# Kernel optimization log

Measured on AMD Instinct MI355X. Metric: run time of the kernel, lower is better.

## Reference

```python
import jax, jax.numpy as jnp
import numpy as np

B, L, D, H, E = 64, 128, 768, 2, 131072  # graphs, nodes/graph, hidden, heads, edges
N = B * L
C = D // H  # per-head channels


def _transformer_conv(x, src, dst, wq, bq, wk, bk, wv, bv, ws, bs):
    # PyG TransformerConv (concat=True, root_weight=True, beta=False)
    n = x.shape[0]
    q = (x @ wq + bq).reshape(n, H, C)
    k = (x @ wk + bk).reshape(n, H, C)
    v = (x @ wv + bv).reshape(n, H, C)
    # per-edge attention logits [E, H]
    logits = jnp.sum(q[dst] * k[src], axis=-1) * (1.0 / np.sqrt(C))
    # scatter softmax over incoming edges of each dst node
    m = jax.ops.segment_max(logits, dst, num_segments=n)
    e = jnp.exp(logits - m[dst])
    s = jax.ops.segment_sum(e, dst, num_segments=n)
    alpha = e / s[dst]  # [E, H]
    msg = alpha[..., None] * v[src]  # [E, H, C]
    agg = jax.ops.segment_sum(msg, dst, num_segments=n).reshape(n, D)
    return agg + x @ ws + bs


def setup_inputs() -> dict:
    key = jax.random.key(0)
    ks = jax.random.split(key, 24)
    x = jax.random.normal(ks[0], (N, D), jnp.float32)
    # within-graph random edges
    dst = jax.random.randint(ks[1], (E,), 0, N)
    off = jax.random.randint(ks[2], (E,), 0, L)
    src = (dst // L) * L + off
    edge_index = jnp.stack([src, dst]).astype(jnp.int32)

    def lin(k, i, o):
        return jax.random.normal(k, (i, o), jnp.float32) * 0.02

    inp = {"x": x, "edge_index": edge_index}
    i = 3
    for layer in ("1", "2"):
        for nm in ("wq", "wk", "wv", "ws"):
            inp[nm + layer] = lin(ks[i], D, D); i += 1
            inp["b" + nm[1] + layer] = jnp.zeros((D,), jnp.float32)
    inp["atti_w"] = lin(ks[i], 2 * D, D); i += 1
    inp["atti_b"] = jnp.zeros((D,), jnp.float32)
    inp["atts_w"] = lin(ks[i], D, 1); i += 1
    inp["atts_b"] = jnp.zeros((1,), jnp.float32)
    inp["fc1_w"] = lin(ks[i], D, D); i += 1
    inp["fc1_b"] = jnp.zeros((D,), jnp.float32)
    inp["fc2_w"] = lin(ks[i], D, 3); i += 1
    inp["fc2_b"] = jnp.zeros((3,), jnp.float32)
    return inp


def reference(x, edge_index, wq1, bq1, wk1, bk1, wv1, bv1, ws1, bs1,
              wq2, bq2, wk2, bk2, wv2, bv2, ws2, bs2,
              atti_w, atti_b, atts_w, atts_b, fc1_w, fc1_b, fc2_w, fc2_b):
    src, dst = edge_index[0], edge_index[1]
    h = jax.nn.relu(_transformer_conv(x, src, dst, wq1, bq1, wk1, bk1, wv1, bv1, ws1, bs1))
    h = jax.nn.relu(_transformer_conv(h, src, dst, wq2, bq2, wk2, bk2, wv2, bv2, ws2, bs2))
    # pad(): equal-size graphs -> reshape, mask all-valid (x_mask all False)
    hp = h.reshape(B, L, D)
    # attention pooling (eval path): query = first node of each graph
    x_q = jnp.broadcast_to(hp[:, :1], hp.shape)  # [B, L, D]
    x_c = jax.nn.relu(jnp.concatenate([x_q, hp], axis=-1) @ atti_w + atti_b)
    score = x_c @ atts_w + atts_b  # [B, L, 1]
    score = jax.nn.softmax(score, axis=1)
    pooled = jnp.sum(hp * score, axis=1)  # [B, D]
    out = jnp.tanh(pooled @ fc1_w + fc1_b) @ fc2_w + fc2_b
    return jax.nn.log_softmax(out, axis=-1)
```

## Files before the change

### kernel.cpp

```cpp
#include <hip/hip_runtime.h>

#define NN 8192
#define DD 768
#define EE 131072
#define BBg 64
#define LLn 128
#define CCh 384

typedef unsigned short u16;
typedef unsigned char u8;
typedef __attribute__((ext_vector_type(8))) short short8;
typedef __attribute__((ext_vector_type(4))) float f32x4;

__device__ __forceinline__ float b2f(u16 u) {
    union { unsigned int i; float f; } x; x.i = ((unsigned int)u) << 16; return x.f;
}
__device__ __forceinline__ u16 f2b(float f) {
    union { float f; unsigned int i; } x; x.f = f;
    unsigned int r = x.i + 0x7fffu + ((x.i >> 16) & 1u);
    return (u16)(r >> 16);
}
__device__ __forceinline__ void gload16(const void* g, void* l) {
    __builtin_amdgcn_global_load_lds((const __attribute__((address_space(1))) void*)g,
                                     (__attribute__((address_space(3))) void*)l, 16, 0, 0);
}

__global__ __launch_bounds__(256) void prep_kernel(const float* __restrict__ in,
                                                   u16* __restrict__ out,
                                                   unsigned int* __restrict__ cnt32,
                                                   float* __restrict__ score) {
    int i = blockIdx.x * 256 + threadIdx.x;
    float4 v = ((const float4*)in)[i];
    ushort4 o; o.x = f2b(v.x); o.y = f2b(v.y); o.z = f2b(v.z); o.w = f2b(v.w);
    ((ushort4*)out)[i] = o;
    if (blockIdx.x < 1024) cnt32[i] = 0;
    else if (blockIdx.x < 1056) score[i - 1024 * 256] = 0.f;
}

struct TP { const float* src; u16* dst; int rowOff; };
struct TP11 { TP a[11]; };

__global__ __launch_bounds__(256) void combo_kernel(TP11 args,
                                                    const int* __restrict__ srcp,
                                                    const int* __restrict__ dstp,
                                                    unsigned int* __restrict__ cnt32) {
    __shared__ float tile[64][65];
    if (blockIdx.z == 11) {
        for (int e = blockIdx.x * 256 + threadIdx.x; e < EE; e += 144 * 256) {
            int d = dstp[e], s = srcp[e];
            int g = d >> 7;
            int idx = (g << 14) + ((d & 127) << 7) + (s & 127);
            atomicAdd(&cnt32[idx >> 2], 1u << ((idx & 3) * 8));
        }
        return;
    }
    TP tp = args.a[blockIdx.z];
    int bx = blockIdx.x % 12, by = blockIdx.x / 12;
    int n0 = bx * 64, k0 = by * 64;
    int t = threadIdx.x;
    int tc = t & 63, tr = t >> 6;
#pragma unroll
    for (int i = 0; i < 16; i++)
        tile[tr + i * 4][tc] = tp.src[(size_t)(tp.rowOff + k0 + tr + i * 4) * DD + n0 + tc];
    __syncthreads();
#pragma unroll
    for (int i = 0; i < 16; i++) {
        int row = tr + i * 4;
        tp.dst[(size_t)(n0 + row) * DD + k0 + tc] = f2b(tile[tc][row]);
    }
}

enum { EPI_F32 = 1, EPI_TANH = 3 };

__global__ __launch_bounds__(256) void gemm_bf16(const u16* __restrict__ A,
                                                 const u16* __restrict__ Wt,
                                                 const float* __restrict__ bias,
                                                 void* __restrict__ outp, int K, int mode) {
    __shared__ u16 As[64][72];
    __shared__ u16 Bs[64][72];
    const int m0 = blockIdx.y * 64, n0 = blockIdx.x * 64;
    const int t = threadIdx.x;
    const int lane = t & 63, w = t >> 6;
    const int tr = t >> 2, tc = (t & 3) * 16;
    f32x4 acc[4] = {{0,0,0,0},{0,0,0,0},{0,0,0,0},{0,0,0,0}};
    const int fRow = lane & 15;
    const int fK = (lane >> 4) * 8;

    for (int k0 = 0; k0 < K; k0 += 64) {
        int4 a0 = *(const int4*)(A + (size_t)(m0 + tr) * K + k0 + tc);
        int4 a1 = *(const int4*)(A + (size_t)(m0 + tr) * K + k0 + tc + 8);
        int4 b0 = *(const int4*)(Wt + (size_t)(n0 + tr) * K + k0 + tc);
        int4 b1 = *(const int4*)(Wt + (size_t)(n0 + tr) * K + k0 + tc + 8);
        __syncthreads();
        *(int4*)&As[tr][tc] = a0; *(int4*)&As[tr][tc + 8] = a1;
        *(int4*)&Bs[tr][tc] = b0; *(int4*)&Bs[tr][tc + 8] = b1;
        __syncthreads();
#pragma unroll
        for (int s = 0; s < 2; s++) {
            short8 af = *(const short8*)&As[w * 16 + fRow][s * 32 + fK];
#pragma unroll
            for (int g = 0; g < 4; g++) {
                short8 bf = *(const short8*)&Bs[g * 16 + fRow][s * 32 + fK];
                acc[g] = __builtin_amdgcn_mfma_f32_16x16x32_bf16(af, bf, acc[g], 0, 0, 0);
            }
        }
    }
    const int colLocal = lane & 15;
    const int rowLocal = (lane >> 4) * 4;
#pragma unroll
    for (int g = 0; g < 4; g++) {
        int col = n0 + g * 16 + colLocal;
        float bv = bias ? bias[col] : 0.f;
#pragma unroll
        for (int i = 0; i < 4; i++) {
            int row = m0 + w * 16 + rowLocal + i;
            float v = acc[g][i] + bv;
            if (mode == EPI_TANH) v = tanhf(v);
            ((float*)outp)[(size_t)row * DD + col] = v;
        }
    }
}

#define SLAB 24576
__global__ __launch_bounds__(512, 2) void gemm256(const u16* __restrict__ A,
                                                  const u16* __restrict__ Wt,
                                                  const float* __restrict__ b0,
                                                  const float* __restrict__ b1,
                                                  const float* __restrict__ b2,
                                                  const float* __restrict__ b3,
                                                  u16* __restrict__ o0, u16* __restrict__ o1,
                                                  u16* __restrict__ o2, u16* __restrict__ o3) {
    __shared__ u16 smem[3 * SLAB];
    const int K = DD;
    const int t = threadIdx.x;
    const int lane = t & 63, w = t >> 6;
    const int wr = w >> 1, wc = w & 1;
    const int id = blockIdx.y * 24 + blockIdx.x;
    const int xcd = id & 7, jj = id >> 3;
    const int by = (xcd >> 1) * 8 + jj / 12;
    const int bx = (xcd & 1) * 12 + jj % 12;
    const int m0 = by * 256, n0 = bx * 128;
    const int fRow = lane & 15, fThr = lane >> 4;
    const u16* Abase = A + (size_t)m0 * K;
    const u16* Bbase = Wt + (size_t)n0 * K;

    auto stage = [&](u16* slab, int kt2) {
        const int k0 = kt2 * 64;
#pragma unroll
        for (int s = 0; s < 4; ++s) {
            int c = t + 512 * s;
            int row = c >> 3;
            int col = ((c & 7) ^ (row & 7)) * 8;
            gload16(Abase + (size_t)row * K + k0 + col, (char*)slab + (size_t)c * 16);
        }
#pragma unroll
        for (int s = 0; s < 2; ++s) {
            int c = t + 512 * s;
            int row = c >> 3;
            int col = ((c & 7) ^ (row & 7)) * 8;
            gload16(Bbase + (size_t)row * K + k0 + col, (char*)(slab + 16384) + (size_t)c * 16);
        }
    };
    auto loadFrags = [&](const u16* As, const u16* Bs, int p, short8* af, short8* bf) {
        const int cj = p * 4 + fThr;
#pragma unroll
        for (int i = 0; i < 4; ++i) {
            const int R = wr * 64 + i * 16 + fRow;
            af[i] = *(const short8*)&As[((size_t)R * 8 + (cj ^ (R & 7))) * 8];
        }
#pragma unroll
        for (int g = 0; g < 4; ++g) {
            const int Rb = wc * 64 + g * 16 + fRow;
            bf[g] = *(const short8*)&Bs[((size_t)Rb * 8 + (cj ^ (Rb & 7))) * 8];
        }
    };

    stage(smem, 0);
    stage(smem + SLAB, 1);
    asm volatile("s_waitcnt vmcnt(6)" ::: "memory");
    __builtin_amdgcn_s_barrier();

    short8 afA[4], bfA[4], afB[4], bfB[4];
    loadFrags(smem, smem + 16384, 0, afA, bfA);

    f32x4 acc[4][4] = {};
    int cur = 0;
    for (int kt = 0; kt < 12; ++kt) {
        const u16* As = smem + cur * SLAB;
        const u16* Bs = As + 16384;
        int nx = cur + 2; if (nx >= 3) nx -= 3;
        int pv = cur + 1; if (pv >= 3) pv -= 3;
        if (kt < 10) stage(smem + nx * SLAB, kt + 2);

        loadFrags(As, Bs, 1, afB, bfB);
        asm volatile("s_waitcnt lgkmcnt(8)" ::: "memory");
        __builtin_amdgcn_sched_barrier(0);
        __builtin_amdgcn_s_setprio(1);
#pragma unroll
        for (int i = 0; i < 4; ++i)
#pragma unroll
            for (int g = 0; g < 4; ++g)
                acc[i][g] = __builtin_amdgcn_mfma_f32_16x16x32_bf16(afA[i], bfA[g], acc[i][g], 0, 0, 0);
        __builtin_amdgcn_s_setprio(0);

        if (kt < 10) asm volatile("s_waitcnt vmcnt(6)" ::: "memory");
        else         asm volatile("s_waitcnt vmcnt(0)" ::: "memory");
        __builtin_amdgcn_s_barrier();

        if (kt < 11) {
            loadFrags(smem + pv * SLAB, smem + pv * SLAB + 16384, 0, afA, bfA);
            asm volatile("s_waitcnt lgkmcnt(8)" ::: "memory");
        } else {
            asm volatile("s_waitcnt lgkmcnt(0)" ::: "memory");
        }
        __builtin_amdgcn_sched_barrier(0);
        __builtin_amdgcn_s_setprio(1);
#pragma unroll
        for (int i = 0; i < 4; ++i)
#pragma unroll
            for (int g = 0; g < 4; ++g)
                acc[i][g] = __builtin_amdgcn_mfma_f32_16x16x32_bf16(afB[i], bfB[g], acc[i][g], 0, 0, 0);
        __builtin_amdgcn_s_setprio(0);
        __builtin_amdgcn_s_barrier();

        cur = pv;
    }

    const int chunk = n0 / DD;
    const float* bp = (chunk == 0) ? b0 : (chunk == 1) ? b1 : (chunk == 2) ? b2 : b3;
    u16* op = (chunk == 0) ? o0 : (chunk == 1) ? o1 : (chunk == 2) ? o2 : o3;
    const int cb0 = n0 - chunk * DD;
    if (chunk == 2) {
        u16 (*Vt)[264] = (u16(*)[264])smem;
#pragma unroll
        for (int g = 0; g < 4; g++) {
            float bv = bp[cb0 + wc * 64 + g * 16 + fRow];
#pragma unroll
            for (int i = 0; i < 4; i++)
#pragma unroll
                for (int rr = 0; rr < 4; rr++)
                    Vt[wc * 64 + g * 16 + fRow][wr * 64 + i * 16 + fThr * 4 + rr] =
                        f2b(acc[i][g][rr] + bv);
        }
        __syncthreads();
#pragma unroll
        for (int ii = 0; ii < 16; ii++) {
            int c = t + 512 * ii;
            int col = c >> 6, ch = c & 63;
            *(ushort4*)(op + (size_t)(cb0 + col) * NN + m0 + ch * 4) =
                *(const ushort4*)&Vt[col][ch * 4];
        }
    } else {
        u16 (*Cs)[136] = (u16(*)[136])smem;
#pragma unroll
        for (int g = 0; g < 4; g++) {
            float bv = bp[cb0 + wc * 64 + g * 16 + fRow];
#pragma unroll
            for (int i = 0; i < 4; i++)
#pragma unroll
                for (int rr = 0; rr < 4; rr++)
                    Cs[wr * 64 + i * 16 + fThr * 4 + rr][wc * 64 + g * 16 + fRow] =
                        f2b(acc[i][g][rr] + bv);
        }
        __syncthreads();
#pragma unroll
        for (int ii = 0; ii < 16; ii++) {
            int c = t + 512 * ii;
            int row = c >> 5, ch = c & 31;
            *(ushort4*)(op + (size_t)(m0 + row) * DD + cb0 + ch * 4) =
                *(const ushort4*)&Cs[row][ch * 4];
        }
    }
}

__global__ __launch_bounds__(256) void gemm_xc(const u16* __restrict__ A,
                                               const u16* __restrict__ Wt,
                                               const u16* __restrict__ wt8,
                                               const float* __restrict__ atti_b,
                                               const float* __restrict__ atts_w,
                                               float* __restrict__ score) {
    __shared__ u16 As[128 * 64];
    __shared__ u16 Bs[128 * 64];
    __shared__ float aq_p[2][128];
    const int K = DD;
    const int t = threadIdx.x;
    const int lane = t & 63, w = t >> 6;
    const int wr = w >> 1, wc = w & 1;
    const int n0 = blockIdx.x * 128, m0 = blockIdx.y * 128;
    const int fRow = lane & 15, fThr = lane >> 4;

    {
        int col = t & 127, kh = t >> 7;
        const u16* xr = A + (size_t)m0 * DD + kh * 384;
        const u16* wr8 = wt8 + (size_t)(n0 + col) * DD + kh * 384;
        float s = 0.f;
#pragma unroll 8
        for (int j = 0; j < 96; j++) {
            ushort4 a4 = *(const ushort4*)(xr + j * 4);
            ushort4 b4 = *(const ushort4*)(wr8 + j * 4);
            s += b2f(a4.x) * b2f(b4.x) + b2f(a4.y) * b2f(b4.y)
               + b2f(a4.z) * b2f(b4.z) + b2f(a4.w) * b2f(b4.w);
        }
        aq_p[kh][col] = s;
    }

    f32x4 acc[4][4] = {};
    const u16* Abase = A + (size_t)m0 * K;
    const u16* Bbase = Wt + (size_t)n0 * K;
    for (int k0 = 0; k0 < K; k0 += 64) {
        __syncthreads();
#pragma unroll
        for (int i = 0; i < 4; i++) {
            int c = t + 256 * i;
            int row = c >> 3;
            int col = ((c & 7) ^ (row & 7)) * 8;
            gload16(Abase + (size_t)row * K + k0 + col, (char*)As + (size_t)c * 16);
            gload16(Bbase + (size_t)row * K + k0 + col, (char*)Bs + (size_t)c * 16);
        }
        __syncthreads();
#pragma unroll
        for (int kk = 0; kk < 64; kk += 32) {
            const int cjW = (kk >> 3) + fThr;
            short8 af[4], bf[4];
#pragma unroll
            for (int i = 0; i < 4; i++) {
                int R = wr * 64 + i * 16 + fRow;
                af[i] = *(const short8*)&As[(R * 8 + (cjW ^ (R & 7))) * 8];
            }
#pragma unroll
            for (int g = 0; g < 4; g++) {
                int R = wc * 64 + g * 16 + fRow;
                bf[g] = *(const short8*)&Bs[(R * 8 + (cjW ^ (R & 7))) * 8];
            }
#pragma unroll
            for (int i = 0; i < 4; i++)
#pragma unroll
                for (int g = 0; g < 4; g++)
                    acc[i][g] = __builtin_amdgcn_mfma_f32_16x16x32_bf16(af[i], bf[g], acc[i][g], 0, 0, 0);
        }
    }
    float rsum[4][4] = {};
#pragma unroll
    for (int g = 0; g < 4; g++) {
        int cl = wc * 64 + g * 16 + fRow;
        int col = n0 + cl;
        float bv = atti_b[col] + aq_p[0][cl] + aq_p[1][cl];
        float av = atts_w[col];
#pragma unroll
        for (int i = 0; i < 4; i++)
#pragma unroll
            for (int rr = 0; rr < 4; rr++) {
                float v = fmaxf(acc[i][g][rr] + bv, 0.f);
                rsum[i][rr] += v * av;
            }
    }
#pragma unroll
    for (int i = 0; i < 4; i++)
#pragma unroll
        for (int rr = 0; rr < 4; rr++) {
            float s = rsum[i][rr];
            s += __shfl_xor(s, 1, 16); s += __shfl_xor(s, 2, 16);
            s += __shfl_xor(s, 4, 16); s += __shfl_xor(s, 8, 16);
            if (fRow == 0)
                atomicAdd(&score[m0 + wr * 64 + i * 16 + fThr * 4 + rr], s);
        }
}

__global__ __launch_bounds__(256) void attn_fused(const u16* __restrict__ qb,
                                                  const u16* __restrict__ kb,
                                                  const u16* __restrict__ vT,
                                                  const u8* __restrict__ cnt,
                                                  const u16* __restrict__ hs,
                                                  u16* __restrict__ out) {
    __shared__ u16 As[64][72];
    __shared__ u16 Bs[128][72];
    __shared__ u16 Pl[64][136];
    __shared__ u16 Vt[64][136];
    const int half = blockIdx.x, hd = blockIdx.y, g = blockIdx.z;
    const int t = threadIdx.x;
    const int lane = t & 63, w = t >> 6;
    const int fRow = lane & 15, fThr = lane >> 4;
    const int dstBase = g * 128 + half * 64;
    const u16* Qb = qb + (size_t)dstBase * DD + hd * CCh;
    const u16* Kb = kb + (size_t)(g * 128) * DD + hd * CCh;

    f32x4 acc[8] = {};
    const int trA = t >> 2, tcA = (t & 3) * 16;
    const int trB = t >> 1, tcB = (t & 1) * 32;
    for (int k0 = 0; k0 < CCh; k0 += 64) {
        int4 a0 = *(const int4*)(Qb + (size_t)trA * DD + k0 + tcA);
        int4 a1 = *(const int4*)(Qb + (size_t)trA * DD + k0 + tcA + 8);
        int4 b0 = *(const int4*)(Kb + (size_t)trB * DD + k0 + tcB);
        int4 b1 = *(const int4*)(Kb + (size_t)trB * DD + k0 + tcB + 8);
        int4 b2 = *(const int4*)(Kb + (size_t)trB * DD + k0 + tcB + 16);
        int4 b3 = *(const int4*)(Kb + (size_t)trB * DD + k0 + tcB + 24);
        __syncthreads();
        *(int4*)&As[trA][tcA] = a0; *(int4*)&As[trA][tcA + 8] = a1;
        *(int4*)&Bs[trB][tcB] = b0; *(int4*)&Bs[trB][tcB + 8] = b1;
        *(int4*)&Bs[trB][tcB + 16] = b2; *(int4*)&Bs[trB][tcB + 24] = b3;
        __syncthreads();
#pragma unroll
        for (int kk = 0; kk < 64; kk += 32) {
            short8 af = *(const short8*)&As[w * 16 + fRow][kk + fThr * 8];
#pragma unroll
            for (int j = 0; j < 8; j++) {
                short8 bf = *(const short8*)&Bs[j * 16 + fRow][kk + fThr * 8];
                acc[j] = __builtin_amdgcn_mfma_f32_16x16x32_bf16(af, bf, acc[j], 0, 0, 0);
            }
        }
    }

    const float scale = 0.05103103630798288f;
    const u8* cg = cnt + ((size_t)g << 14);
    const int rbase = half * 64 + w * 16 + fThr * 4;
    float pv[8][4];
#pragma unroll
    for (int i = 0; i < 4; i++) {
        float m = -3.4e38f;
#pragma unroll
        for (int j = 0; j < 8; j++) {
            float c = (float)cg[(rbase + i) * 128 + j * 16 + fRow];
            float s = acc[j][i] * scale;
            pv[j][i] = c;
            if (c > 0.f) m = fmaxf(m, s);
        }
#pragma unroll
        for (int msk = 1; msk <= 8; msk <<= 1) m = fmaxf(m, __shfl_xor(m, msk, 16));
        float sum = 0.f;
#pragma unroll
        for (int j = 0; j < 8; j++) {
            float p = (pv[j][i] > 0.f) ? pv[j][i] * __expf(acc[j][i] * scale - m) : 0.f;
            pv[j][i] = p; sum += p;
        }
#pragma unroll
        for (int msk = 1; msk <= 8; msk <<= 1) sum += __shfl_xor(sum, msk, 16);
        float inv = (sum > 0.f) ? 1.f / sum : 0.f;
#pragma unroll
        for (int j = 0; j < 8; j++)
            Pl[w * 16 + fThr * 4 + i][j * 16 + fRow] = f2b(pv[j][i] * inv);
    }

    for (int cc = 0; cc < 6; cc++) {
        __syncthreads();
#pragma unroll
        for (int ii = 0; ii < 4; ii++) {
            int q = t + 256 * ii;
            int row = q >> 4, col = (q & 15) * 8;
            *(int4*)&Vt[row][col] =
                *(const int4*)(vT + (size_t)(hd * CCh + cc * 64 + row) * NN + g * 128 + col);
        }
        __syncthreads();
        f32x4 acc2[4] = {};
#pragma unroll
        for (int kk = 0; kk < 128; kk += 32) {
            short8 af = *(const short8*)&Pl[w * 16 + fRow][kk + fThr * 8];
#pragma unroll
            for (int j = 0; j < 4; j++) {
                short8 bf = *(const short8*)&Vt[j * 16 + fRow][kk + fThr * 8];
                acc2[j] = __builtin_amdgcn_mfma_f32_16x16x32_bf16(af, bf, acc2[j], 0, 0, 0);
            }
        }
#pragma unroll
        for (int j = 0; j < 4; j++) {
            int c = hd * CCh + cc * 64 + j * 16 + fRow;
#pragma unroll
            for (int i = 0; i < 4; i++) {
                int row = dstBase + w * 16 + fThr * 4 + i;
                size_t idx = (size_t)row * DD + c;
                float r = fmaxf(acc2[j][i] + b2f(hs[idx]), 0.f);
                out[idx] = f2b(r);
            }
        }
    }
}

__global__ __launch_bounds__(192) void pool_kernel(const float* __restrict__ score,
                                                   const u16* __restrict__ hx,
                                                   u16* __restrict__ pb) {
    int b = blockIdx.x, t = threadIdx.x;
    __shared__ float sprob[LLn];
    if (t < 64) {
        float s0 = score[b * LLn + t];
        float s1 = score[b * LLn + 64 + t];
        float mx = fmaxf(s0, s1);
#pragma unroll
        for (int m = 1; m <= 32; m <<= 1) mx = fmaxf(mx, __shfl_xor(mx, m, 64));
        float e0 = __expf(s0 - mx), e1 = __expf(s1 - mx);
        float sum = e0 + e1;
#pragma unroll
        for (int m = 1; m <= 32; m <<= 1) sum += __shfl_xor(sum, m, 64);
        float inv = 1.f / sum;
        sprob[t] = e0 * inv; sprob[t + 64] = e1 * inv;
    }
    __syncthreads();
    int c = t * 4;
    float a0 = 0, a1 = 0, a2 = 0, a3 = 0;
    for (int l = 0; l < LLn; l++) {
        float wl = sprob[l];
        ushort4 hv = *(const ushort4*)(hx + (size_t)(b * LLn + l) * DD + c);
        a0 += wl * b2f(hv.x); a1 += wl * b2f(hv.y); a2 += wl * b2f(hv.z); a3 += wl * b2f(hv.w);
    }
    ushort4 o; o.x = f2b(a0); o.y = f2b(a1); o.z = f2b(a2); o.w = f2b(a3);
    *(ushort4*)(pb + (size_t)b * DD + c) = o;
}

__global__ __launch_bounds__(256) void head2_kernel(const float* __restrict__ u,
                                                    const float* __restrict__ fc2w,
                                                    const float* __restrict__ fc2b,
                                                    float* __restrict__ outp) {
    int b = blockIdx.x, t = threadIdx.x;
    __shared__ float sred[4][3];
    float p0 = 0, p1 = 0, p2 = 0;
    for (int k = t; k < DD; k += 256) {
        float uv = u[(size_t)b * DD + k];
        p0 += uv * fc2w[k * 3 + 0]; p1 += uv * fc2w[k * 3 + 1]; p2 += uv * fc2w[k * 3 + 2];
    }
#pragma unroll
    for (int m = 1; m <= 32; m <<= 1) {
        p0 += __shfl_xor(p0, m, 64); p1 += __shfl_xor(p1, m, 64); p2 += __shfl_xor(p2, m, 64);
    }
    int w = t >> 6, lane = t & 63;
    if (lane == 0) { sred[w][0] = p0; sred[w][1] = p1; sred[w][2] = p2; }
    __syncthreads();
    if (t == 0) {
        float z0 = fc2b[0], z1 = fc2b[1], z2 = fc2b[2];
        for (int i = 0; i < 4; i++) { z0 += sred[i][0]; z1 += sred[i][1]; z2 += sred[i][2]; }
        float mx = fmaxf(z0, fmaxf(z1, z2));
        float lse = mx + logf(__expf(z0 - mx) + __expf(z1 - mx) + __expf(z2 - mx));
        outp[b * 3 + 0] = z0 - lse; outp[b * 3 + 1] = z1 - lse; outp[b * 3 + 2] = z2 - lse;
    }
}

static inline char* carve(char*& p, size_t bytes) {
    char* r = p;
    p += (bytes + 255) & ~(size_t)255;
    return r;
}

extern "C" void kernel_launch(void* const* d_in, const int* in_sizes, int n_in,
                              void* d_out, int out_size, void* d_ws, size_t ws_size,
                              hipStream_t stream) {
    const float* x = (const float*)d_in[0];
    const int* ei = (const int*)d_in[1];
    const int* srcp = ei;
    const int* dstp = ei + EE;
    const float* wL[8] = {(const float*)d_in[2], (const float*)d_in[4], (const float*)d_in[6],
                          (const float*)d_in[8], (const float*)d_in[10], (const float*)d_in[12],
                          (const float*)d_in[14], (const float*)d_in[16]};
    const float* bL[8] = {(const float*)d_in[3], (const float*)d_in[5], (const float*)d_in[7],
                          (const float*)d_in[9], (const float*)d_in[11], (const float*)d_in[13],
                          (const float*)d_in[15], (const float*)d_in[17]};
    const float* atti_w = (const float*)d_in[18];
    const float* atti_b = (const float*)d_in[19];
    const float* atts_w = (const float*)d_in[20];
    const float* fc1_w = (const float*)d_in[22];
    const float* fc1_b = (const float*)d_in[23];
    const float* fc2_w = (const float*)d_in[24];
    const float* fc2_b = (const float*)d_in[25];
    float* outp = (float*)d_out;

    char* p = (char*)d_ws;
    const size_t ndb = (size_t)NN * DD * 2;
    const size_t wsz = (size_t)DD * DD * 2;
    u16* qb = (u16*)carve(p, ndb);
    u16* kb = (u16*)carve(p, ndb);
    u16* vt = (u16*)carve(p, ndb);
    u16* xb = (u16*)carve(p, ndb);
    u16* hb = (u16*)carve(p, ndb);
    u16* hs = (u16*)carve(p, ndb);
    u16* wtcat1 = (u16*)carve(p, wsz * 4);
    u16* wtcat2 = (u16*)carve(p, wsz * 4);
    u16* wt8 = (u16*)carve(p, wsz);
    u16* wt9 = (u16*)carve(p, wsz);
    u16* wtfc1 = (u16*)carve(p, wsz);
    u16* pb = (u16*)carve(p, (size_t)BBg * DD * 2);
    float* uu = (float*)carve(p, (size_t)BBg * DD * 4);
    u8* cnt = (u8*)carve(p, (size_t)BBg * 128 * 128);
    float* score = (float*)carve(p, NN * 4);

    prep_kernel<<<6144, 256, 0, stream>>>(x, xb, (unsigned int*)cnt, score);

    TP11 tps;
    for (int i = 0; i < 4; i++) tps.a[i] = {wL[i], wtcat1 + (size_t)i * DD * DD, 0};
    for (int i = 0; i < 4; i++) tps.a[4 + i] = {wL[4 + i], wtcat2 + (size_t)i * DD * DD, 0};
    tps.a[8] = {atti_w, wt8, 0};
    tps.a[9] = {atti_w, wt9, DD};
    tps.a[10] = {fc1_w, wtfc1, 0};
    combo_kernel<<<dim3(144, 1, 12), 256, 0, stream>>>(tps, srcp, dstp, (unsigned int*)cnt);

    dim3 gf(24, 32);
    dim3 ga(2, 2, BBg);
    gemm256<<<gf, 512, 0, stream>>>(xb, wtcat1, bL[0], bL[1], bL[2], bL[3], qb, kb, vt, hs);
    attn_fused<<<ga, 256, 0, stream>>>(qb, kb, vt, cnt, hs, hb);
    gemm256<<<gf, 512, 0, stream>>>(hb, wtcat2, bL[4], bL[5], bL[6], bL[7], qb, kb, vt, hs);
    attn_fused<<<ga, 256, 0, stream>>>(qb, kb, vt, cnt, hs, xb);

    gemm_xc<<<dim3(6, 64), 256, 0, stream>>>(xb, wt9, wt8, atti_b, atts_w, score);

    pool_kernel<<<BBg, 192, 0, stream>>>(score, xb, pb);
    gemm_bf16<<<dim3(12, 1), 256, 0, stream>>>(pb, wtfc1, fc1_b, uu, DD, EPI_TANH);
    head2_kernel<<<BBg, 256, 0, stream>>>(uu, fc2_w, fc2_b, outp);
}
```

Measured before the change: 343.2 us.

## Split K across wave pairs in gemm256 with LDS cross-wave reduction

Reworks the projection GEMM so that each pair of waves splits the K dimension of every 64-wide tile instead of splitting the N columns. Each wave accumulates a 64x128 partial tile, and the two partials are summed through LDS before the bias and store epilogue. The global-to-LDS staging is split into two halves interleaved with the MFMA phases. This is meant to cut B-fragment LDS reads per MFMA and to overlap loads with compute better, at the cost of doubled accumulator registers (risking occupancy at 2 blocks per CU) and an extra LDS reduction pass.

Result: no change. 344.0 us (+0.2%).

```diff
diff --git a/kernel.cpp b/kernel.cpp
--- a/kernel.cpp
+++ b/kernel.cpp
@@ -134,7 +134,7 @@
     const int K = DD;
     const int t = threadIdx.x;
     const int lane = t & 63, w = t >> 6;
-    const int wr = w >> 1, wc = w & 1;
+    const int mrow = w >> 1, ks = w & 1;
     const int id = blockIdx.y * 24 + blockIdx.x;
     const int xcd = id & 7, jj = id >> 3;
     const int by = (xcd >> 1) * 8 + jj / 12;
@@ -144,87 +144,162 @@
     const u16* Abase = A + (size_t)m0 * K;
     const u16* Bbase = Wt + (size_t)n0 * K;
 
-    auto stage = [&](u16* slab, int kt2) {
-        const int k0 = kt2 * 64;
-#pragma unroll
-        for (int s = 0; s < 4; ++s) {
-            int c = t + 512 * s;
-            int row = c >> 3;
-            int col = ((c & 7) ^ (row & 7)) * 8;
-            gload16(Abase + (size_t)row * K + k0 + col, (char*)slab + (size_t)c * 16);
-        }
-#pragma unroll
-        for (int s = 0; s < 2; ++s) {
-            int c = t + 512 * s;
-            int row = c >> 3;
-            int col = ((c & 7) ^ (row & 7)) * 8;
-            gload16(Bbase + (size_t)row * K + k0 + col, (char*)(slab + 16384) + (size_t)c * 16);
+    auto stageH = [&](u16* slab, int ktS, int half) {
+        const int k0 = ktS * 64;
+        if (half == 0) {
+#pragma unroll
+            for (int s = 0; s < 3; ++s) {
+                int c = t + 512 * s;
+                int row = c >> 3, col = ((c & 7) ^ (row & 7)) * 8;
+                gload16(Abase + (size_t)row * K + k0 + col, (char*)slab + (size_t)c * 16);
+            }
+        } else {
+            {
+                int c = t + 512 * 3;
+                int row = c >> 3, col = ((c & 7) ^ (row & 7)) * 8;
+                gload16(Abase + (size_t)row * K + k0 + col, (char*)slab + (size_t)c * 16);
+            }
+#pragma unroll
+            for (int s = 0; s < 2; ++s) {
+                int c = t + 512 * s;
+                int row = c >> 3, col = ((c & 7) ^ (row & 7)) * 8;
+                gload16(Bbase + (size_t)row * K + k0 + col, (char*)(slab + 16384) + (size_t)c * 16);
+            }
         }
     };
-    auto loadFrags = [&](const u16* As, const u16* Bs, int p, short8* af, short8* bf) {
-        const int cj = p * 4 + fThr;
+    auto loadAB = [&](const u16* As, short8 (&af)[4], short8 (&bfLo)[4]) {
+        const u16* Bs = As + 16384;
+        const int cj = ks * 4 + fThr;
 #pragma unroll
         for (int i = 0; i < 4; ++i) {
-            const int R = wr * 64 + i * 16 + fRow;
+            int R = mrow * 64 + i * 16 + fRow;
             af[i] = *(const short8*)&As[((size_t)R * 8 + (cj ^ (R & 7))) * 8];
         }
 #pragma unroll
         for (int g = 0; g < 4; ++g) {
-            const int Rb = wc * 64 + g * 16 + fRow;
+            int Rb = g * 16 + fRow;
+            bfLo[g] = *(const short8*)&Bs[((size_t)Rb * 8 + (cj ^ (Rb & 7))) * 8];
+        }
+    };
+    auto loadHi = [&](const u16* As, short8 (&bf)[4]) {
+        const u16* Bs = As + 16384;
+        const int cj = ks * 4 + fThr;
+#pragma unroll
+        for (int g = 0; g < 4; ++g) {
+            int Rb = (g + 4) * 16 + fRow;
             bf[g] = *(const short8*)&Bs[((size_t)Rb * 8 + (cj ^ (Rb & 7))) * 8];
         }
     };
 
-    stage(smem, 0);
-    stage(smem + SLAB, 1);
-    asm volatile("s_waitcnt vmcnt(6)" ::: "memory");
-    __builtin_amdgcn_s_barrier();
-
-    short8 afA[4], bfA[4], afB[4], bfB[4];
-    loadFrags(smem, smem + 16384, 0, afA, bfA);
-
-    f32x4 acc[4][4] = {};
-    int cur = 0;
-    for (int kt = 0; kt < 12; ++kt) {
-        const u16* As = smem + cur * SLAB;
-        const u16* Bs = As + 16384;
-        int nx = cur + 2; if (nx >= 3) nx -= 3;
-        int pv = cur + 1; if (pv >= 3) pv -= 3;
-        if (kt < 10) stage(smem + nx * SLAB, kt + 2);
-
-        loadFrags(As, Bs, 1, afB, bfB);
-        asm volatile("s_waitcnt lgkmcnt(8)" ::: "memory");
+    f32x4 acc[4][8] = {};
+    auto mfmaLo = [&](short8 (&af)[4], short8 (&bf)[4]) {
+#pragma unroll
+        for (int i = 0; i < 4; ++i)
+#pragma unroll
+            for (int g = 0; g < 4; ++g)
+                acc[i][g] = __builtin_amdgcn_mfma_f32_16x16x32_bf16(af[i], bf[g], acc[i][g], 0, 0, 0);
+    };
+    auto mfmaHi = [&](short8 (&af)[4], short8 (&bf)[4]) {
+#pragma unroll
+        for (int i = 0; i < 4; ++i)
+#pragma unroll
+            for (int g = 0; g < 4; ++g)
+                acc[i][4 + g] = __builtin_amdgcn_mfma_f32_16x16x32_bf16(af[i], bf[g], acc[i][4 + g], 0, 0, 0);
+    };
+
+    short8 afP[4], bfLoP[4], afQ[4], bfLoQ[4], bfH[4];
+
+    auto tileStep = [&](const u16* As, const u16* AsN, u16* Sst,
+                        short8 (&af)[4], short8 (&bfLo)[4],
+                        short8 (&afN)[4], short8 (&bfLoN)[4], int kt) {
+        loadHi(As, bfH);
+        if (kt <= 9) stageH(Sst, kt + 2, 0);
+        asm volatile("s_waitcnt lgkmcnt(4)" ::: "memory");
         __builtin_amdgcn_sched_barrier(0);
         __builtin_amdgcn_s_setprio(1);
-#pragma unroll
-        for (int i = 0; i < 4; ++i)
-#pragma unroll
-            for (int g = 0; g < 4; ++g)
-                acc[i][g] = __builtin_amdgcn_mfma_f32_16x16x32_bf16(afA[i], bfA[g], acc[i][g], 0, 0, 0);
+        mfmaLo(af, bfLo);
         __builtin_amdgcn_s_setprio(0);
-
-        if (kt < 10) asm volatile("s_waitcnt vmcnt(6)" ::: "memory");
+        if (kt <= 9) asm volatile("s_waitcnt vmcnt(3)" ::: "memory");
         else         asm volatile("s_waitcnt vmcnt(0)" ::: "memory");
         __builtin_amdgcn_s_barrier();
-
-        if (kt < 11) {
-            loadFrags(smem + pv * SLAB, smem + pv * SLAB + 16384, 0, afA, bfA);
+        if (kt <= 10) {
+            loadAB(AsN, afN, bfLoN);
+            if (kt <= 9) stageH(Sst, kt + 2, 1);
             asm volatile("s_waitcnt lgkmcnt(8)" ::: "memory");
         } else {
             asm volatile("s_waitcnt lgkmcnt(0)" ::: "memory");
         }
         __builtin_amdgcn_sched_barrier(0);
         __builtin_amdgcn_s_setprio(1);
-#pragma unroll
-        for (int i = 0; i < 4; ++i)
-#pragma unroll
-            for (int g = 0; g < 4; ++g)
-                acc[i][g] = __builtin_amdgcn_mfma_f32_16x16x32_bf16(afB[i], bfB[g], acc[i][g], 0, 0, 0);
+        mfmaHi(af, bfH);
         __builtin_amdgcn_s_setprio(0);
         __builtin_amdgcn_s_barrier();
-
-        cur = pv;
-    }
+    };
+
+    stageH(smem, 0, 0); stageH(smem, 0, 1);
+    stageH(smem + SLAB, 1, 0); stageH(smem + SLAB, 1, 1);
+    asm volatile("s_waitcnt vmcnt(6)" ::: "memory");
+    __builtin_amdgcn_s_barrier();
+    loadAB(smem, afP, bfLoP);
+
+    int cur = 0;
+    for (int it = 0; it < 6; ++it) {
+        int s1 = cur + 1; if (s1 >= 3) s1 -= 3;
+        int s2 = cur + 2; if (s2 >= 3) s2 -= 3;
+        u16* S0 = smem + cur * SLAB;
+        u16* S1 = smem + s1 * SLAB;
+        u16* S2 = smem + s2 * SLAB;
+        tileStep(S0, S1, S2, afP, bfLoP, afQ, bfLoQ, 2 * it);
+        tileStep(S1, S2, S0, afQ, bfLoQ, afP, bfLoP, 2 * it + 1);
+        cur = s2;
+    }
+
+    char* xbuf = (char*)smem;
+    const int wreg = mrow * 2 + 1 - ks;
+    const int rreg = mrow * 2 + ks;
+    if (ks == 0) {
+#pragma unroll
+        for (int i = 0; i < 4; i++)
+#pragma unroll
+            for (int g = 0; g < 4; g++) {
+                int f = i * 4 + g;
+                int unit = lane * 16 + ((f + lane) & 15);
+                *(f32x4*)(xbuf + wreg * 16384 + unit * 16) = acc[i][4 + g];
+            }
+    } else {
+#pragma unroll
+        for (int i = 0; i < 4; i++)
+#pragma unroll
+            for (int g = 0; g < 4; g++) {
+                int f = i * 4 + g;
+                int unit = lane * 16 + ((f + lane) & 15);
+                *(f32x4*)(xbuf + wreg * 16384 + unit * 16) = acc[i][g];
+            }
+    }
+    __syncthreads();
+    f32x4 fin[4][4];
+    if (ks == 0) {
+#pragma unroll
+        for (int i = 0; i < 4; i++)
+#pragma unroll
+            for (int g = 0; g < 4; g++) {
+                int f = i * 4 + g;
+                int unit = lane * 16 + ((f + lane) & 15);
+                f32x4 p = *(const f32x4*)(xbuf + rreg * 16384 + unit * 16);
+                fin[i][g] = acc[i][g] + p;
+            }
+    } else {
+#pragma unroll
+        for (int i = 0; i < 4; i++)
+#pragma unroll
+            for (int g = 0; g < 4; g++) {
+                int f = i * 4 + g;
+                int unit = lane * 16 + ((f + lane) & 15);
+                f32x4 p = *(const f32x4*)(xbuf + rreg * 16384 + unit * 16);
+                fin[i][g] = acc[i][4 + g] + p;
+            }
+    }
+    __syncthreads();
 
     const int chunk = n0 / DD;
     const float* bp = (chunk == 0) ? b0 : (chunk == 1) ? b1 : (chunk == 2) ? b2 : b3;
@@ -234,13 +309,13 @@
         u16 (*Vt)[264] = (u16(*)[264])smem;
 #pragma unroll
         for (int g = 0; g < 4; g++) {
-            float bv = bp[cb0 + wc * 64 + g * 16 + fRow];
+            float bv = bp[cb0 + ks * 64 + g * 16 + fRow];
 #pragma unroll
             for (int i = 0; i < 4; i++)
 #pragma unroll
                 for (int rr = 0; rr < 4; rr++)
-                    Vt[wc * 64 + g * 16 + fRow][wr * 64 + i * 16 + fThr * 4 + rr] =
-                        f2b(acc[i][g][rr] + bv);
+                    Vt[ks * 64 + g * 16 + fRow][mrow * 64 + i * 16 + fThr * 4 + rr] =
+                        f2b(fin[i][g][rr] + bv);
         }
         __syncthreads();
 #pragma unroll
@@ -254,13 +329,13 @@
         u16 (*Cs)[136] = (u16(*)[136])smem;
 #pragma unroll
         for (int g = 0; g < 4; g++) {
-            float bv = bp[cb0 + wc * 64 + g * 16 + fRow];
+            float bv = bp[cb0 + ks * 64 + g * 16 + fRow];
 #pragma unroll
             for (int i = 0; i < 4; i++)
 #pragma unroll
                 for (int rr = 0; rr < 4; rr++)
-                    Cs[wr * 64 + i * 16 + fThr * 4 + rr][wc * 64 + g * 16 + fRow] =
-                        f2b(acc[i][g][rr] + bv);
+                    Cs[mrow * 64 + i * 16 + fThr * 4 + rr][ks * 64 + g * 16 + fRow] =
+                        f2b(fin[i][g][rr] + bv);
         }
         __syncthreads();
 #pragma unroll
```

## Enlarge QKVS GEMM tile to 256x256 with double-buffered quarter-step pipeline

Applied to the files above, without the earlier changes.

Changes the fused Q/K/V/skip projection GEMM from 256x128 output tiles with a triple-buffered K loop to 256x256 tiles. Each wave now owns 128x64 of the output, and the loads for the next K tile are split into four sub-stages interleaved with four MFMA sub-blocks over two shared-memory buffers. The larger tile raises arithmetic intensity and halves the number of blocks, from 768 to 384. In exchange, the 128 accumulator registers per thread add register pressure at 2 blocks/CU, there are more barriers per K step, and the epilogue now runs in two shared-memory passes.

Measured after the change: 368.5 us. 1.07x slower.

```diff
diff --git a/kernel.cpp b/kernel.cpp
--- a/kernel.cpp
+++ b/kernel.cpp
@@ -121,7 +121,7 @@
     }
 }
 
-#define SLAB 24576
+#define BUFU 32768
 __global__ __launch_bounds__(512, 2) void gemm256(const u16* __restrict__ A,
                                                   const u16* __restrict__ Wt,
                                                   const float* __restrict__ b0,
@@ -130,145 +130,192 @@
                                                   const float* __restrict__ b3,
                                                   u16* __restrict__ o0, u16* __restrict__ o1,
                                                   u16* __restrict__ o2, u16* __restrict__ o3) {
-    __shared__ u16 smem[3 * SLAB];
+    __shared__ u16 smem[2 * BUFU];
     const int K = DD;
     const int t = threadIdx.x;
     const int lane = t & 63, w = t >> 6;
-    const int wr = w >> 1, wc = w & 1;
-    const int id = blockIdx.y * 24 + blockIdx.x;
+    const int wm = w >> 2, wn = w & 3;
+    const int id = blockIdx.y * 12 + blockIdx.x;
     const int xcd = id & 7, jj = id >> 3;
-    const int by = (xcd >> 1) * 8 + jj / 12;
-    const int bx = (xcd & 1) * 12 + jj % 12;
-    const int m0 = by * 256, n0 = bx * 128;
+    const int by = xcd * 4 + jj / 12;
+    const int bx = jj % 12;
+    const int m0 = by * 256, n0 = bx * 256;
     const int fRow = lane & 15, fThr = lane >> 4;
     const u16* Abase = A + (size_t)m0 * K;
     const u16* Bbase = Wt + (size_t)n0 * K;
 
-    auto stage = [&](u16* slab, int kt2) {
-        const int k0 = kt2 * 64;
-#pragma unroll
-        for (int s = 0; s < 4; ++s) {
-            int c = t + 512 * s;
-            int row = c >> 3;
-            int col = ((c & 7) ^ (row & 7)) * 8;
-            gload16(Abase + (size_t)row * K + k0 + col, (char*)slab + (size_t)c * 16);
-        }
+    auto stageA = [&](int b, int kt, int h) {
+        const int k0 = kt * 64;
+        char* dst = (char*)(smem + b * BUFU);
 #pragma unroll
         for (int s = 0; s < 2; ++s) {
-            int c = t + 512 * s;
-            int row = c >> 3;
-            int col = ((c & 7) ^ (row & 7)) * 8;
-            gload16(Bbase + (size_t)row * K + k0 + col, (char*)(slab + 16384) + (size_t)c * 16);
+            int c = h * 1024 + t + 512 * s;
+            int row = c >> 3, col = ((c & 7) ^ (row & 7)) * 8;
+            gload16(Abase + (size_t)row * K + k0 + col, dst + (size_t)c * 16);
         }
     };
-    auto loadFrags = [&](const u16* As, const u16* Bs, int p, short8* af, short8* bf) {
-        const int cj = p * 4 + fThr;
-#pragma unroll
-        for (int i = 0; i < 4; ++i) {
-            const int R = wr * 64 + i * 16 + fRow;
-            af[i] = *(const short8*)&As[((size_t)R * 8 + (cj ^ (R & 7))) * 8];
-        }
-#pragma unroll
-        for (int g = 0; g < 4; ++g) {
-            const int Rb = wc * 64 + g * 16 + fRow;
-            bf[g] = *(const short8*)&Bs[((size_t)Rb * 8 + (cj ^ (Rb & 7))) * 8];
+    auto stageB = [&](int b, int kt, int h) {
+        const int k0 = kt * 64;
+        char* dst = (char*)(smem + b * BUFU + 16384);
+#pragma unroll
+        for (int s = 0; s < 2; ++s) {
+            int c = h * 1024 + t + 512 * s;
+            int row = c >> 3, col = ((c & 7) ^ (row & 7)) * 8;
+            gload16(Bbase + (size_t)row * K + k0 + col, dst + (size_t)c * 16);
         }
     };
 
-    stage(smem, 0);
-    stage(smem + SLAB, 1);
-    asm volatile("s_waitcnt vmcnt(6)" ::: "memory");
-    __builtin_amdgcn_s_barrier();
-
-    short8 afA[4], bfA[4], afB[4], bfB[4];
-    loadFrags(smem, smem + 16384, 0, afA, bfA);
-
-    f32x4 acc[4][4] = {};
-    int cur = 0;
-    for (int kt = 0; kt < 12; ++kt) {
-        const u16* As = smem + cur * SLAB;
-        const u16* Bs = As + 16384;
-        int nx = cur + 2; if (nx >= 3) nx -= 3;
-        int pv = cur + 1; if (pv >= 3) pv -= 3;
-        if (kt < 10) stage(smem + nx * SLAB, kt + 2);
-
-        loadFrags(As, Bs, 1, afB, bfB);
-        asm volatile("s_waitcnt lgkmcnt(8)" ::: "memory");
+    short8 fa[4][2], fb0[2][2], fb1[2][2];
+    f32x4 acc[8][4] = {};
+
+    auto loadA = [&](const u16* Ab, int ih) {
+#pragma unroll
+        for (int i = 0; i < 4; ++i)
+#pragma unroll
+            for (int kk = 0; kk < 2; ++kk) {
+                int R = wm * 128 + ih * 64 + i * 16 + fRow;
+                int cj = kk * 4 + fThr;
+                fa[i][kk] = *(const short8*)&Ab[((size_t)R * 8 + (cj ^ (R & 7))) * 8];
+            }
+    };
+    auto loadB = [&](const u16* Bb, int gh, short8 (&fb)[2][2]) {
+#pragma unroll
+        for (int g = 0; g < 2; ++g)
+#pragma unroll
+            for (int kk = 0; kk < 2; ++kk) {
+                int Rb = wn * 64 + gh * 32 + g * 16 + fRow;
+                int cj = kk * 4 + fThr;
+                fb[g][kk] = *(const short8*)&Bb[((size_t)Rb * 8 + (cj ^ (Rb & 7))) * 8];
+            }
+    };
+    auto mm = [&](int ibase, short8 (&fb)[2][2], int gbase) {
+#pragma unroll
+        for (int kk = 0; kk < 2; ++kk)
+#pragma unroll
+            for (int i = 0; i < 4; ++i)
+#pragma unroll
+                for (int g = 0; g < 2; ++g)
+                    acc[ibase + i][gbase + g] = __builtin_amdgcn_mfma_f32_16x16x32_bf16(
+                        fa[i][kk], fb[g][kk], acc[ibase + i][gbase + g], 0, 0, 0);
+    };
+
+    auto ktile4 = [&](int bufb, auto&& st1, auto&& st2, auto&& st3, auto&& st4, bool vm0end) {
+        const u16* Ab = smem + bufb * BUFU;
+        const u16* Bb = Ab + 16384;
+        loadA(Ab, 0);
+        loadB(Bb, 0, fb0);
+        st1();
+        __builtin_amdgcn_s_barrier();
+        asm volatile("s_waitcnt lgkmcnt(0)" ::: "memory");
         __builtin_amdgcn_sched_barrier(0);
         __builtin_amdgcn_s_setprio(1);
-#pragma unroll
-        for (int i = 0; i < 4; ++i)
-#pragma unroll
-            for (int g = 0; g < 4; ++g)
-                acc[i][g] = __builtin_amdgcn_mfma_f32_16x16x32_bf16(afA[i], bfA[g], acc[i][g], 0, 0, 0);
+        mm(0, fb0, 0);
         __builtin_amdgcn_s_setprio(0);
-
-        if (kt < 10) asm volatile("s_waitcnt vmcnt(6)" ::: "memory");
-        else         asm volatile("s_waitcnt vmcnt(0)" ::: "memory");
-        __builtin_amdgcn_s_barrier();
-
-        if (kt < 11) {
-            loadFrags(smem + pv * SLAB, smem + pv * SLAB + 16384, 0, afA, bfA);
-            asm volatile("s_waitcnt lgkmcnt(8)" ::: "memory");
-        } else {
-            asm volatile("s_waitcnt lgkmcnt(0)" ::: "memory");
-        }
+        __builtin_amdgcn_s_barrier();
+        loadB(Bb, 1, fb1);
+        st2();
+        __builtin_amdgcn_s_barrier();
+        asm volatile("s_waitcnt lgkmcnt(0)" ::: "memory");
         __builtin_amdgcn_sched_barrier(0);
         __builtin_amdgcn_s_setprio(1);
-#pragma unroll
-        for (int i = 0; i < 4; ++i)
-#pragma unroll
-            for (int g = 0; g < 4; ++g)
-                acc[i][g] = __builtin_amdgcn_mfma_f32_16x16x32_bf16(afB[i], bfB[g], acc[i][g], 0, 0, 0);
+        mm(0, fb1, 2);
         __builtin_amdgcn_s_setprio(0);
         __builtin_amdgcn_s_barrier();
-
-        cur = pv;
-    }
-
-    const int chunk = n0 / DD;
+        loadA(Ab, 1);
+        st3();
+        __builtin_amdgcn_s_barrier();
+        asm volatile("s_waitcnt lgkmcnt(0)" ::: "memory");
+        __builtin_amdgcn_sched_barrier(0);
+        __builtin_amdgcn_s_setprio(1);
+        mm(4, fb1, 2);
+        __builtin_amdgcn_s_setprio(0);
+        __builtin_amdgcn_s_barrier();
+        st4();
+        __builtin_amdgcn_s_barrier();
+        __builtin_amdgcn_sched_barrier(0);
+        __builtin_amdgcn_s_setprio(1);
+        mm(4, fb0, 0);
+        __builtin_amdgcn_s_setprio(0);
+        if (vm0end) asm volatile("s_waitcnt vmcnt(0)" ::: "memory");
+        else        asm volatile("s_waitcnt vmcnt(4)" ::: "memory");
+        __builtin_amdgcn_s_barrier();
+    };
+
+    stageB(0, 0, 0); stageB(0, 0, 1);
+    stageA(0, 0, 0); stageA(0, 0, 1);
+    stageB(1, 1, 0); stageB(1, 1, 1);
+    asm volatile("s_waitcnt vmcnt(4)" ::: "memory");
+    __builtin_amdgcn_s_barrier();
+
+    for (int it = 0; it < 6; ++it) {
+        const int T2 = 2 * it + 2, T3 = 2 * it + 3;
+        ktile4(0,
+               [&] { stageA(1, 2 * it + 1, 0); },
+               [&] { stageA(1, 2 * it + 1, 1); },
+               [&] { if (T2 < 12) stageB(0, T2, 0); },
+               [&] { if (T2 < 12) stageB(0, T2, 1); },
+               it == 5);
+        ktile4(1,
+               [&] { if (T2 < 12) stageA(0, T2, 0); },
+               [&] { if (T2 < 12) stageA(0, T2, 1); },
+               [&] { if (T3 < 12) stageB(1, T3, 0); },
+               [&] { if (T3 < 12) stageB(1, T3, 1); },
+               false);
+    }
+
+    const int chunk = bx / 3;
     const float* bp = (chunk == 0) ? b0 : (chunk == 1) ? b1 : (chunk == 2) ? b2 : b3;
     u16* op = (chunk == 0) ? o0 : (chunk == 1) ? o1 : (chunk == 2) ? o2 : o3;
-    const int cb0 = n0 - chunk * DD;
+    const int cb0 = (bx % 3) * 256;
+    u16 (*Cs)[264] = (u16(*)[264])smem;
     if (chunk == 2) {
-        u16 (*Vt)[264] = (u16(*)[264])smem;
-#pragma unroll
-        for (int g = 0; g < 4; g++) {
-            float bv = bp[cb0 + wc * 64 + g * 16 + fRow];
-#pragma unroll
-            for (int i = 0; i < 4; i++)
-#pragma unroll
-                for (int rr = 0; rr < 4; rr++)
-                    Vt[wc * 64 + g * 16 + fRow][wr * 64 + i * 16 + fThr * 4 + rr] =
-                        f2b(acc[i][g][rr] + bv);
-        }
-        __syncthreads();
-#pragma unroll
-        for (int ii = 0; ii < 16; ii++) {
-            int c = t + 512 * ii;
-            int col = c >> 6, ch = c & 63;
-            *(ushort4*)(op + (size_t)(cb0 + col) * NN + m0 + ch * 4) =
-                *(const ushort4*)&Vt[col][ch * 4];
+        for (int q = 0; q < 2; ++q) {
+            __syncthreads();
+            if ((wn >> 1) == q) {
+#pragma unroll
+                for (int g = 0; g < 4; ++g) {
+                    int colL = (wn & 1) * 64 + g * 16 + fRow;
+                    float bv = bp[cb0 + q * 128 + colL];
+#pragma unroll
+                    for (int i = 0; i < 8; ++i)
+#pragma unroll
+                        for (int rr = 0; rr < 4; ++rr)
+                            Cs[colL][wm * 128 + i * 16 + fThr * 4 + rr] =
+                                f2b(acc[i][g][rr] + bv);
+                }
+            }
+            __syncthreads();
+#pragma unroll
+            for (int ii = 0; ii < 16; ++ii) {
+                int c = t + 512 * ii;
+                int col = c >> 6, ch = c & 63;
+                *(ushort4*)(op + (size_t)(cb0 + q * 128 + col) * NN + m0 + ch * 4) =
+                    *(const ushort4*)&Cs[col][ch * 4];
+            }
         }
     } else {
-        u16 (*Cs)[136] = (u16(*)[136])smem;
-#pragma unroll
-        for (int g = 0; g < 4; g++) {
-            float bv = bp[cb0 + wc * 64 + g * 16 + fRow];
-#pragma unroll
-            for (int i = 0; i < 4; i++)
-#pragma unroll
-                for (int rr = 0; rr < 4; rr++)
-                    Cs[wr * 64 + i * 16 + fThr * 4 + rr][wc * 64 + g * 16 + fRow] =
-                        f2b(acc[i][g][rr] + bv);
-        }
-        __syncthreads();
-#pragma unroll
-        for (int ii = 0; ii < 16; ii++) {
-            int c = t + 512 * ii;
-            int row = c >> 5, ch = c & 31;
-            *(ushort4*)(op + (size_t)(m0 + row) * DD + cb0 + ch * 4) =
-                *(const ushort4*)&Cs[row][ch * 4];
+        for (int p = 0; p < 2; ++p) {
+            __syncthreads();
+            if (wm == p) {
+#pragma unroll
+                for (int g = 0; g < 4; ++g) {
+                    int col = wn * 64 + g * 16 + fRow;
+                    float bv = bp[cb0 + col];
+#pragma unroll
+                    for (int i = 0; i < 8; ++i)
+#pragma unroll
+                        for (int rr = 0; rr < 4; ++rr)
+                            Cs[i * 16 + fThr * 4 + rr][col] = f2b(acc[i][g][rr] + bv);
+                }
+            }
+            __syncthreads();
+#pragma unroll
+            for (int ii = 0; ii < 16; ++ii) {
+                int c = t + 512 * ii;
+                int row = c >> 6, ch = c & 63;
+                *(ushort4*)(op + (size_t)(m0 + p * 128 + row) * DD + cb0 + ch * 4) =
+                    *(const ushort4*)&Cs[row][ch * 4];
+            }
         }
     }
 }
@@ -588,7 +635,7 @@
     tps.a[10] = {fc1_w, wtfc1, 0};
     combo_kernel<<<dim3(144, 1, 12), 256, 0, stream>>>(tps, srcp, dstp, (unsigned int*)cnt);
 
-    dim3 gf(24, 32);
+    dim3 gf(12, 32);
     dim3 ga(2, 2, BBg);
     gemm256<<<gf, 512, 0, stream>>>(xb, wtcat1, bL[0], bL[1], bL[2], bL[3], qb, kb, vt, hs);
     attn_fused<<<ga, 256, 0, stream>>>(qb, kb, vt, cnt, hs, hb);
```
